# Optimization experiments

Hardware: AMD Instinct MI355X
Metric: run time of the kernel (lower is better)

Reference implementation:

```python
import jax, jax.numpy as jnp
import numpy as np

B, W, H, L, D = 4, 32, 32, 32, 256
K, S, V = 24, 16384, 8  # heads, selected positions per head, logits per head
N = B * W * H * L


def setup_inputs() -> dict:
    key = jax.random.key(0)
    k1, k2, k3, k4, k5 = jax.random.split(key, 5)
    block_type_grid = jax.random.randint(k1, (B, W, H, L), 0, 800, dtype=jnp.int32)
    features = jax.random.normal(k2, (B, W, H, L, D), dtype=jnp.float32)
    mask_idx = jax.random.randint(k3, (K, S), 0, N, dtype=jnp.int32)
    head_weights = jax.random.normal(k4, (K, D, V), dtype=jnp.float32) * (1.0 / np.sqrt(D))
    head_bias = jax.random.normal(k5, (K, V), dtype=jnp.float32) * 0.01
    return {
        "block_type_grid": block_type_grid,
        "features": features,
        "mask_idx": mask_idx,
        "head_weights": head_weights,
        "head_bias": head_bias,
    }


def reference(block_type_grid, features, mask_idx, head_weights, head_bias):
    # Flatten spatial grid: (B,W,H,L,D) -> (N,D)
    feats_flat = features.reshape(-1, D)
    # Grouped boolean-mask gather (as fixed-size index gather): (K,S,D)
    gathered = feats_flat[mask_idx]
    # Per-head small Linear: logits[k,s,v] = gathered[k,s,:] @ W[k,:,v] + b[k,v]
    logits = jnp.einsum('ksd,kdv->ksv', gathered, head_weights) + head_bias[:, None, :]
    return logits
```

## Files before the change

### kernel.cpp

```cpp
#include <hip/hip_runtime.h>


#define KH 24
#define SS 16384
#define VV 8
#define DD 256
#define NG 192
#define NROWS 131072

typedef short bf16x8 __attribute__((ext_vector_type(8)));
typedef float f32x4  __attribute__((ext_vector_type(4)));
typedef int   i32x4  __attribute__((ext_vector_type(4)));

__device__ __forceinline__ unsigned short f32_bf16_rne(float f) {
    unsigned u = __builtin_bit_cast(unsigned, f);
    u = (u + 0x7FFFu + ((u >> 16) & 1u)) >> 16;
    return (unsigned short)u;
}

__device__ __forceinline__ unsigned pack_bf16x2(float lo, float hi) {
    unsigned ulo = __builtin_bit_cast(unsigned, lo) + 0x8000u;
    unsigned uhi = __builtin_bit_cast(unsigned, hi) + 0x8000u;
    return __builtin_amdgcn_perm(uhi, ulo, 0x07060302);
}

__global__ __launch_bounds__(256, 3) void dense_logits_kernel(
    const float* __restrict__ feats,
    const float* __restrict__ head_w,
    const float* __restrict__ head_b,
    unsigned short* __restrict__ logits)
{
    const int lane = threadIdx.x & 63;
    const int wv   = threadIdx.x >> 6;
    const int n    = lane & 15;
    const int q    = lane >> 4;

    bf16x8 Bf[3][8];
    float  bias_v[3];
#pragma unroll
    for (int tile = 0; tile < 3; ++tile) {
        const int n_g = wv * 48 + tile * 16 + n;
        const float* Wh = head_w + (size_t)(n_g >> 3) * (DD * VV) + (n_g & 7);
#pragma unroll
        for (int t = 0; t < 8; ++t)
#pragma unroll
            for (int j = 0; j < 8; ++j)
                Bf[tile][t][j] = (short)f32_bf16_rne(Wh[(t * 32 + q * 8 + j) * VV]);
        bias_v[tile] = head_b[(n_g >> 3) * VV + (n_g & 7)];
    }

    const int rbase = blockIdx.x * 256;
#pragma unroll 1
    for (int mt = 0; mt < 16; ++mt) {
        const int mbase = rbase + mt * 16;
        const float* p = feats + (size_t)(mbase + n) * DD + q * 8;

        f32x4 acc[3];
#pragma unroll
        for (int tile = 0; tile < 3; ++tile) {
            const float b = bias_v[tile];
            acc[tile][0] = b; acc[tile][1] = b; acc[tile][2] = b; acc[tile][3] = b;
        }
#pragma unroll
        for (int t = 0; t < 8; ++t) {
            const float4 a0 = *(const float4*)(p + t * 32);
            const float4 a1 = *(const float4*)(p + t * 32 + 4);
            i32x4 ai;
            ai[0] = (int)pack_bf16x2(a0.x, a0.y);
            ai[1] = (int)pack_bf16x2(a0.z, a0.w);
            ai[2] = (int)pack_bf16x2(a1.x, a1.y);
            ai[3] = (int)pack_bf16x2(a1.z, a1.w);
            const bf16x8 a = __builtin_bit_cast(bf16x8, ai);
            acc[0] = __builtin_amdgcn_mfma_f32_16x16x32_bf16(a, Bf[0][t], acc[0], 0, 0, 0);
            acc[1] = __builtin_amdgcn_mfma_f32_16x16x32_bf16(a, Bf[1][t], acc[1], 0, 0, 0);
            acc[2] = __builtin_amdgcn_mfma_f32_16x16x32_bf16(a, Bf[2][t], acc[2], 0, 0, 0);
        }
#pragma unroll
        for (int tile = 0; tile < 3; ++tile) {
            const int n_g = wv * 48 + tile * 16 + n;
            unsigned short* op = logits + (size_t)(mbase + q * 4) * NG + n_g;
#pragma unroll
            for (int i = 0; i < 4; ++i)
                op[(size_t)i * NG] = f32_bf16_rne(acc[tile][i]);
        }
    }
}

__global__ __launch_bounds__(256) void gather_logits_kernel(
    const unsigned short* __restrict__ logits,
    const int* __restrict__ mask_idx,
    float* __restrict__ out)
{
    const int tid  = blockIdx.x * 256 + threadIdx.x;
    const int gsel = tid >> 1;
    const int half = tid & 1;
    const int k    = gsel >> 14;
    const int idx  = mask_idx[gsel];
    const unsigned short* lp = logits + (size_t)idx * NG + k * VV + half * 4;
    const ushort4 u = *(const ushort4*)lp;
    float4 r;
    r.x = __builtin_bit_cast(float, (unsigned)u.x << 16);
    r.y = __builtin_bit_cast(float, (unsigned)u.y << 16);
    r.z = __builtin_bit_cast(float, (unsigned)u.z << 16);
    r.w = __builtin_bit_cast(float, (unsigned)u.w << 16);
    *(float4*)(out + (size_t)gsel * VV + half * 4) = r;
}

template <int CTRL>
__device__ __forceinline__ float dpp_mov(float x) {
    int xi = __builtin_bit_cast(int, x);
    int r = __builtin_amdgcn_update_dpp(xi, xi, CTRL, 0xF, 0xF, false);
    return __builtin_bit_cast(float, r);
}

__device__ __forceinline__ float reduce8(const float acc[8], int lane) {
    const bool b0 = lane & 1;
    const bool b1 = lane & 2;
    const bool b2 = lane & 4;
    float a4[4];
#pragma unroll
    for (int j = 0; j < 4; ++j) {
        const float keep = b0 ? acc[2 * j + 1] : acc[2 * j];
        const float send = b0 ? acc[2 * j] : acc[2 * j + 1];
        a4[j] = keep + dpp_mov<0xB1>(send);
    }
    float a2[2];
#pragma unroll
    for (int m = 0; m < 2; ++m) {
        const float keep = b1 ? a4[2 * m + 1] : a4[2 * m];
        const float send = b1 ? a4[2 * m] : a4[2 * m + 1];
        a2[m] = keep + dpp_mov<0x4E>(send);
    }
    const float keep = b2 ? a2[1] : a2[0];
    const float send = b2 ? a2[0] : a2[1];
    float a1 = keep + __shfl_xor(send, 4, 64);
    a1 += dpp_mov<0x128>(a1);
    a1 += __shfl_xor(a1, 16, 64);
    a1 += __shfl_xor(a1, 32, 64);
    return a1;
}

__global__ __launch_bounds__(256) void attr_decoder_fallback(
    const float* __restrict__ feats, const int* __restrict__ mask_idx,
    const float* __restrict__ head_w, const float* __restrict__ head_b,
    float* __restrict__ out)
{
    const int lane  = threadIdx.x & 63;
    const int wvv   = threadIdx.x >> 6;
    const int k     = blockIdx.x >> 7;
    const int chunk = blockIdx.x & 127;
    const float* Wk = head_w + (size_t)k * (DD * VV);
    float w[4][8];
#pragma unroll
    for (int t = 0; t < 4; ++t) {
        const float4 a = *(const float4*)(Wk + (lane * 4 + t) * VV);
        const float4 b = *(const float4*)(Wk + (lane * 4 + t) * VV + 4);
        w[t][0] = a.x; w[t][1] = a.y; w[t][2] = a.z; w[t][3] = a.w;
        w[t][4] = b.x; w[t][5] = b.y; w[t][6] = b.z; w[t][7] = b.w;
    }
    const float bias = head_b[k * VV + (lane & 7)];
    const float4* feats4 = (const float4*)feats;
    const int s_base = chunk * 128 + wvv * 32;
    const int* mi = mask_idx + k * SS + s_base;
    float* outp = out + ((size_t)k * SS + s_base) * VV;
    const int g = (lane >> 3) & 3;
    for (int i = 0; i < 32; i += 4) {
        const int4 rows = *(const int4*)(mi + i);
        const float4 f0 = feats4[(size_t)rows.x * 64 + lane];
        const float4 f1 = feats4[(size_t)rows.y * 64 + lane];
        const float4 f2 = feats4[(size_t)rows.z * 64 + lane];
        const float4 f3 = feats4[(size_t)rows.w * 64 + lane];
        float r[4];
        const float4 f[4] = {f0, f1, f2, f3};
#pragma unroll
        for (int u = 0; u < 4; ++u) {
            float acc[8];
#pragma unroll
            for (int v = 0; v < 8; ++v) {
                acc[v] = f[u].x * w[0][v];
                acc[v] = fmaf(f[u].y, w[1][v], acc[v]);
                acc[v] = fmaf(f[u].z, w[2][v], acc[v]);
                acc[v] = fmaf(f[u].w, w[3][v], acc[v]);
            }
            r[u] = reduce8(acc, lane);
        }
        const float r01 = (g & 1) ? r[1] : r[0];
        const float r23 = (g & 1) ? r[3] : r[2];
        const float val = ((g & 2) ? r23 : r01) + bias;
        if (lane < 32) outp[i * VV + lane] = val;
    }
}

extern "C" void kernel_launch(void* const* d_in, const int* in_sizes, int n_in,
                              void* d_out, int out_size, void* d_ws, size_t ws_size,
                              hipStream_t stream) {
    const float* feats    = (const float*)d_in[1];
    const int*   mask_idx = (const int*)  d_in[2];
    const float* head_w   = (const float*)d_in[3];
    const float* head_b   = (const float*)d_in[4];
    float* out = (float*)d_out;

    const size_t need = (size_t)NROWS * NG * sizeof(unsigned short);
    if (ws_size >= need) {
        unsigned short* logits = (unsigned short*)d_ws;
        dense_logits_kernel<<<dim3(NROWS / 256), dim3(256), 0, stream>>>(
            feats, head_w, head_b, logits);
        gather_logits_kernel<<<dim3(KH * SS * 2 / 256), dim3(256), 0, stream>>>(
            logits, mask_idx, out);
    } else {
        attr_decoder_fallback<<<dim3(KH * 128), dim3(256), 0, stream>>>(
            feats, mask_idx, head_w, head_b, out);
    }
}
```

Baseline: 283.8 us.

## Split dense logits over column groups and store packed row-quad layout

After: 347.0 us. +22.3%, slower.

```diff
diff --git a/kernel.cpp b/kernel.cpp
--- a/kernel.cpp
+++ b/kernel.cpp
@@ -10,12 +10,10 @@
 
 typedef short bf16x8 __attribute__((ext_vector_type(8)));
 typedef float f32x4  __attribute__((ext_vector_type(4)));
-typedef int   i32x4  __attribute__((ext_vector_type(4)));
-
-__device__ __forceinline__ unsigned short f32_bf16_rne(float f) {
+
+__device__ __forceinline__ unsigned short f32_bf16_rhu(float f) {
     unsigned u = __builtin_bit_cast(unsigned, f);
-    u = (u + 0x7FFFu + ((u >> 16) & 1u)) >> 16;
-    return (unsigned short)u;
+    return (unsigned short)((u + 0x8000u) >> 16);
 }
 
 __device__ __forceinline__ unsigned pack_bf16x2(float lo, float hi) {
@@ -24,7 +22,11 @@
     return __builtin_amdgcn_perm(uhi, ulo, 0x07060302);
 }
 
-__global__ __launch_bounds__(256, 3) void dense_logits_kernel(
+__device__ __forceinline__ float bf2f(unsigned short s) {
+    return __builtin_bit_cast(float, (unsigned)s << 16);
+}
+
+__global__ __launch_bounds__(256, 4) void dense_logits_kernel(
     const float* __restrict__ feats,
     const float* __restrict__ head_w,
     const float* __restrict__ head_b,
@@ -35,54 +37,43 @@
     const int n    = lane & 15;
     const int q    = lane >> 4;
 
-    bf16x8 Bf[3][8];
-    float  bias_v[3];
-#pragma unroll
-    for (int tile = 0; tile < 3; ++tile) {
-        const int n_g = wv * 48 + tile * 16 + n;
-        const float* Wh = head_w + (size_t)(n_g >> 3) * (DD * VV) + (n_g & 7);
-#pragma unroll
-        for (int t = 0; t < 8; ++t)
-#pragma unroll
-            for (int j = 0; j < 8; ++j)
-                Bf[tile][t][j] = (short)f32_bf16_rne(Wh[(t * 32 + q * 8 + j) * VV]);
-        bias_v[tile] = head_b[(n_g >> 3) * VV + (n_g & 7)];
-    }
-
-    const int rbase = blockIdx.x * 256;
+    const int g  = blockIdx.x / 512;
+    const int rb = blockIdx.x % 512;
+    const int n_g = g * 64 + wv * 16 + n;
+
+    const float* Wh = head_w + (size_t)(n_g >> 3) * (DD * VV) + (n_g & 7);
+    bf16x8 Bf[8];
+#pragma unroll
+    for (int t = 0; t < 8; ++t)
+#pragma unroll
+        for (int j = 0; j < 8; ++j)
+            Bf[t][j] = (short)f32_bf16_rhu(Wh[(size_t)(t * 32 + q * 8 + j) * VV]);
+    const float bias = head_b[(n_g >> 3) * VV + (n_g & 7)];
+
+    const int rbase = rb * 256;
 #pragma unroll 1
     for (int mt = 0; mt < 16; ++mt) {
         const int mbase = rbase + mt * 16;
         const float* p = feats + (size_t)(mbase + n) * DD + q * 8;
 
-        f32x4 acc[3];
-#pragma unroll
-        for (int tile = 0; tile < 3; ++tile) {
-            const float b = bias_v[tile];
-            acc[tile][0] = b; acc[tile][1] = b; acc[tile][2] = b; acc[tile][3] = b;
-        }
+        f32x4 acc = {bias, bias, bias, bias};
 #pragma unroll
         for (int t = 0; t < 8; ++t) {
             const float4 a0 = *(const float4*)(p + t * 32);
             const float4 a1 = *(const float4*)(p + t * 32 + 4);
-            i32x4 ai;
+            int ai[4];
             ai[0] = (int)pack_bf16x2(a0.x, a0.y);
             ai[1] = (int)pack_bf16x2(a0.z, a0.w);
             ai[2] = (int)pack_bf16x2(a1.x, a1.y);
             ai[3] = (int)pack_bf16x2(a1.z, a1.w);
-            const bf16x8 a = __builtin_bit_cast(bf16x8, ai);
-            acc[0] = __builtin_amdgcn_mfma_f32_16x16x32_bf16(a, Bf[0][t], acc[0], 0, 0, 0);
-            acc[1] = __builtin_amdgcn_mfma_f32_16x16x32_bf16(a, Bf[1][t], acc[1], 0, 0, 0);
-            acc[2] = __builtin_amdgcn_mfma_f32_16x16x32_bf16(a, Bf[2][t], acc[2], 0, 0, 0);
+            const bf16x8 a = __builtin_bit_cast(bf16x8, *(const int4*)ai);
+            acc = __builtin_amdgcn_mfma_f32_16x16x32_bf16(a, Bf[t], acc, 0, 0, 0);
         }
-#pragma unroll
-        for (int tile = 0; tile < 3; ++tile) {
-            const int n_g = wv * 48 + tile * 16 + n;
-            unsigned short* op = logits + (size_t)(mbase + q * 4) * NG + n_g;
-#pragma unroll
-            for (int i = 0; i < 4; ++i)
-                op[(size_t)i * NG] = f32_bf16_rne(acc[tile][i]);
-        }
+        int2 pk;
+        pk.x = (int)pack_bf16x2(acc[0], acc[1]);
+        pk.y = (int)pack_bf16x2(acc[2], acc[3]);
+        unsigned short* op = logits + ((size_t)((mbase >> 2) + q) * NG + n_g) * 4;
+        *(int2*)op = pk;
     }
 }
 
@@ -96,13 +87,13 @@
     const int half = tid & 1;
     const int k    = gsel >> 14;
     const int idx  = mask_idx[gsel];
-    const unsigned short* lp = logits + (size_t)idx * NG + k * VV + half * 4;
-    const ushort4 u = *(const ushort4*)lp;
+    const unsigned short* p =
+        logits + (size_t)(idx >> 2) * (NG * 4) + (size_t)(k * VV + half * 4) * 4 + (idx & 3);
     float4 r;
-    r.x = __builtin_bit_cast(float, (unsigned)u.x << 16);
-    r.y = __builtin_bit_cast(float, (unsigned)u.y << 16);
-    r.z = __builtin_bit_cast(float, (unsigned)u.z << 16);
-    r.w = __builtin_bit_cast(float, (unsigned)u.w << 16);
+    r.x = bf2f(p[0]);
+    r.y = bf2f(p[4]);
+    r.z = bf2f(p[8]);
+    r.w = bf2f(p[12]);
     *(float4*)(out + (size_t)gsel * VV + half * 4) = r;
 }
 
@@ -203,7 +194,7 @@
     const size_t need = (size_t)NROWS * NG * sizeof(unsigned short);
     if (ws_size >= need) {
         unsigned short* logits = (unsigned short*)d_ws;
-        dense_logits_kernel<<<dim3(NROWS / 256), dim3(256), 0, stream>>>(
+        dense_logits_kernel<<<dim3(3 * 512), dim3(256), 0, stream>>>(
             feats, head_w, head_b, logits);
         gather_logits_kernel<<<dim3(KH * SS * 2 / 256), dim3(256), 0, stream>>>(
             logits, mask_idx, out);
```
